# Kernel optimization log

Measured on AMD Instinct MI355X. Metric: run time of the kernel, lower is better.

Reference implementation:

```python
import jax, jax.numpy as jnp
import numpy as np

ALPHA = 0.5
N_NODES = 100000
N_EDGES = 1600000
D_IN = 128
D_OUT = 128


def setup_inputs() -> dict:
    key = jax.random.key(0)
    k1, k2, k3, k4, k5, k6 = jax.random.split(key, 6)
    x = jax.random.normal(k1, (N_NODES, D_IN), dtype=jnp.float32)
    edge_index = jax.random.randint(k2, (2, N_EDGES), 0, N_NODES, dtype=jnp.int64)
    # torch Linear default init: U(-1/sqrt(fan_in), 1/sqrt(fan_in)); scale similar here
    s = 1.0 / np.sqrt(D_IN)
    W_src = jax.random.uniform(k3, (D_OUT, D_IN), jnp.float32, -s, s)
    b_src = jax.random.uniform(k4, (D_OUT,), jnp.float32, -s, s)
    W_dst = jax.random.uniform(k5, (D_OUT, D_IN), jnp.float32, -s, s)
    b_dst = jax.random.uniform(k6, (D_OUT,), jnp.float32, -s, s)
    return {"x": x, "edge_index": edge_index, "W_src": W_src, "b_src": b_src,
            "W_dst": W_dst, "b_dst": b_dst}


def _inv_sqrt(deg):
    # deg^{-1/2} with inf -> 0 (isolated nodes)
    return jnp.where(deg > 0, jax.lax.rsqrt(jnp.maximum(deg, 1e-30)), 0.0)


def reference(x, edge_index, W_src, b_src, W_dst, b_dst):
    n = x.shape[0]
    row, col = edge_index[0], edge_index[1]
    ones = jnp.ones(row.shape[0], dtype=x.dtype)
    # degrees of directed adjacency A[row, col] = 1
    deg_out = jax.ops.segment_sum(ones, row, num_segments=n)  # row sums
    deg_in = jax.ops.segment_sum(ones, col, num_segments=n)   # col sums
    # D_out^{-1/2} A D_in^{-1/2} edge weights; transpose norm yields the SAME weights
    w = _inv_sqrt(deg_out)[row] * _inv_sqrt(deg_in)[col]      # [E]
    # adj_norm @ x : aggregate sources (col) into destinations (row)
    agg_fwd = jax.ops.segment_sum(w[:, None] * x[col], row, num_segments=n)  # [N, D_IN]
    # adj_t_norm @ x : aggregate destinations (row) into sources (col)
    agg_bwd = jax.ops.segment_sum(w[:, None] * x[row], col, num_segments=n)  # [N, D_IN]
    out = ALPHA * (agg_fwd @ W_src.T + b_src) + (1.0 - ALPHA) * (agg_bwd @ W_dst.T + b_dst)
    return out
```

## Files before the change

kernel.cpp:

```cpp
#include <hip/hip_runtime.h>
#include <stdint.h>

#define D 128
#define CE 2048
#define CAP 5120

typedef __attribute__((ext_vector_type(8))) __bf16 bf16x8;
typedef __attribute__((ext_vector_type(4))) float floatx4;

union FragU { uint4 u; bf16x8 b; };

__device__ __forceinline__ float bf16_lo(uint32_t u) { return __uint_as_float(u << 16); }
__device__ __forceinline__ float bf16_hi(uint32_t u) { return __uint_as_float(u & 0xffff0000u); }
__device__ __forceinline__ uint16_t f32_to_bf16(float f) {
    uint32_t u = __float_as_uint(f);
    uint32_t r = u + 0x7fffu + ((u >> 16) & 1u);
    return (uint16_t)(r >> 16);
}
__device__ __forceinline__ uint32_t pack2(float a, float b) {
    return (uint32_t)f32_to_bf16(a) | ((uint32_t)f32_to_bf16(b) << 16);
}

__global__ __launch_bounds__(256) void k_init(uint32_t* __restrict__ gcursor, int nb2)
{
    for (int j = threadIdx.x + blockIdx.x * 256; j < nb2; j += gridDim.x * 256)
        gcursor[j] = (uint32_t)j * CAP;
}

__global__ __launch_bounds__(256) void k_part(
    const int* __restrict__ ei, int E, int nbuk,
    uint32_t* __restrict__ gcursor, uint32_t* __restrict__ gpairs)
{
    __shared__ uint32_t cnt[1024];
    __shared__ uint32_t loff[1024];
    __shared__ uint32_t gbase[1024];
    __shared__ uint32_t spair[2 * CE];
    __shared__ uint16_t sbid[2 * CE];
    __shared__ uint32_t ssum[256];
    int nb2 = 2 * nbuk;
    for (int j = threadIdx.x; j < nb2; j += 256) cnt[j] = 0;
    __syncthreads();
    int base = blockIdx.x * CE;
    int lim = min(CE, E - base);
    for (int i = threadIdx.x; i < lim; i += 256) {
        int r = ei[base + i];
        int c = ei[E + base + i];
        atomicAdd(&cnt[r >> 8], 1u);
        atomicAdd(&cnt[nbuk + (c >> 8)], 1u);
    }
    __syncthreads();
    uint32_t v0 = 0, v1 = 0, v2 = 0, v3 = 0;
    int b0 = threadIdx.x * 4;
    if (b0 < nb2)     v0 = cnt[b0];
    if (b0 + 1 < nb2) v1 = cnt[b0 + 1];
    if (b0 + 2 < nb2) v2 = cnt[b0 + 2];
    if (b0 + 3 < nb2) v3 = cnt[b0 + 3];
    uint32_t tsum = v0 + v1 + v2 + v3;
    ssum[threadIdx.x] = tsum;
    __syncthreads();
    for (int off = 1; off < 256; off <<= 1) {
        uint32_t t = (threadIdx.x >= (unsigned)off) ? ssum[threadIdx.x - off] : 0u;
        __syncthreads();
        ssum[threadIdx.x] += t;
        __syncthreads();
    }
    uint32_t run = ssum[threadIdx.x] - tsum;
    if (b0 < nb2)     loff[b0]     = run;
    if (b0 + 1 < nb2) loff[b0 + 1] = run + v0;
    if (b0 + 2 < nb2) loff[b0 + 2] = run + v0 + v1;
    if (b0 + 3 < nb2) loff[b0 + 3] = run + v0 + v1 + v2;
    __syncthreads();
    for (int j = threadIdx.x; j < nb2; j += 256) {
        uint32_t c2 = cnt[j];
        gbase[j] = c2 ? atomicAdd(&gcursor[j], c2) : 0u;
        cnt[j] = loff[j];
    }
    __syncthreads();
    for (int i = threadIdx.x; i < lim; i += 256) {
        int r = ei[base + i];
        int c = ei[E + base + i];
        int bf = r >> 8;
        uint32_t sf = atomicAdd(&cnt[bf], 1u);
        spair[sf] = ((uint32_t)c << 8) | (uint32_t)(r & 255);
        sbid[sf] = (uint16_t)bf;
        int bb = nbuk + (c >> 8);
        uint32_t sb = atomicAdd(&cnt[bb], 1u);
        spair[sb] = ((uint32_t)r << 8) | (uint32_t)(c & 255);
        sbid[sb] = (uint16_t)bb;
    }
    __syncthreads();
    int total = 2 * lim;
    for (int s2 = threadIdx.x; s2 < total; s2 += 256) {
        int b = sbid[s2];
        gpairs[gbase[b] + ((uint32_t)s2 - loff[b])] = spair[s2];
    }
}

__global__ __launch_bounds__(256) void k_build(
    const uint32_t* __restrict__ gpairs, const uint32_t* __restrict__ gcursor,
    int nbuk, int N,
    int* __restrict__ edata, uint32_t* __restrict__ ptrg, uint32_t* __restrict__ degg,
    float* __restrict__ inv_o, float* __restrict__ inv_i)
{
    __shared__ uint32_t hist[256], cur[256], ssum[256];
    int b = blockIdx.x;
    int dir = (b >= nbuk) ? 1 : 0;
    int node0 = (b - dir * nbuk) << 8;
    uint32_t base = (uint32_t)b * CAP;
    uint32_t cnt_b = gcursor[b] - base;
    hist[threadIdx.x] = 0;
    __syncthreads();
    for (uint32_t i = threadIdx.x; i < cnt_b; i += 256)
        atomicAdd(&hist[gpairs[base + i] & 255u], 1u);
    __syncthreads();
    uint32_t h = hist[threadIdx.x];
    ssum[threadIdx.x] = h;
    __syncthreads();
    for (int off = 1; off < 256; off <<= 1) {
        uint32_t t = (threadIdx.x >= (unsigned)off) ? ssum[threadIdx.x - off] : 0u;
        __syncthreads();
        ssum[threadIdx.x] += t;
        __syncthreads();
    }
    uint32_t excl = ssum[threadIdx.x] - h;
    cur[threadIdx.x] = excl;
    int n = node0 + threadIdx.x;
    if (n < N) {
        ptrg[dir * N + n] = base + excl;
        degg[dir * N + n] = h;
        float iv = h ? rsqrtf((float)h) : 0.0f;
        if (dir == 0) inv_o[n] = iv; else inv_i[n] = iv;
    }
    __syncthreads();
    for (uint32_t i = threadIdx.x; i < cnt_b; i += 256) {
        uint32_t e = gpairs[base + i];
        uint32_t pos = atomicAdd(&cur[e & 255u], 1u);
        edata[base + pos] = (int)(e >> 8);
    }
}

__global__ __launch_bounds__(256) void k_mm(
    const float* __restrict__ x,
    const float* __restrict__ Wsrc, const float* __restrict__ Wdst,
    const float* __restrict__ inv_o, const float* __restrict__ inv_i,
    uint32_t* __restrict__ u2, uint32_t* __restrict__ v2, int N)
{
    __shared__ uint4 sWf[2048];
    const int lane = threadIdx.x & 63;
    const int m16 = lane & 15;
    const int quad = lane >> 4;
    const int mat = blockIdx.x & 1;
    uint32_t* outb = mat ? v2 : u2;
    const float* inv = mat ? inv_o : inv_i;
    const float* Wm = mat ? Wdst : Wsrc;

    {
        uint32_t* sW32 = (uint32_t*)sWf;
        for (int idx = threadIdx.x; idx < 8192; idx += 256) {
            int slot = idx >> 2, j2 = idx & 3;
            int ct = slot >> 8, ks = (slot >> 6) & 3, qd = (slot >> 4) & 3, mm = slot & 15;
            const float2 w = *(const float2*)(Wm + (ct * 16 + mm) * 128 + ks * 32 + qd * 8 + 2 * j2);
            sW32[idx] = pack2(0.5f * w.x, 0.5f * w.y);
        }
    }
    __syncthreads();

    const int ntiles = (N + 15) >> 4;
    const int wslot = (blockIdx.x >> 1) * 4 + (threadIdx.x >> 6);
    const int nslot = (gridDim.x >> 1) * 4;

    for (int t = wslot; t < ntiles; t += nslot) {
        int node = t * 16 + m16;
        int rowA = node < N ? node : N - 1;
        const float4* xr = (const float4*)(x + (long)rowA * 128);
        bf16x8 Xf[4];
        #pragma unroll
        for (int ks = 0; ks < 4; ++ks) {
            float4 p0 = xr[ks * 8 + quad * 2];
            float4 p1 = xr[ks * 8 + quad * 2 + 1];
            FragU f;
            f.u.x = pack2(p0.x, p0.y);
            f.u.y = pack2(p0.z, p0.w);
            f.u.z = pack2(p1.x, p1.y);
            f.u.w = pack2(p1.z, p1.w);
            Xf[ks] = f.b;
        }
        float iv = inv[rowA];
        bool ok = (node < N);
        #pragma unroll
        for (int ct = 0; ct < 8; ++ct) {
            floatx4 acc = {};
            #pragma unroll
            for (int ks = 0; ks < 4; ++ks) {
                FragU wf; wf.u = sWf[ct * 256 + ks * 64 + lane];
                acc = __builtin_amdgcn_mfma_f32_16x16x32_bf16(wf.b, Xf[ks], acc, 0, 0, 0);
            }
            if (ok) {
                uint2 val;
                val.x = pack2(acc[0] * iv, acc[1] * iv);
                val.y = pack2(acc[2] * iv, acc[3] * iv);
                *(uint2*)(outb + (long)node * 64 + ct * 8 + quad * 2) = val;
            }
        }
    }
}

__global__ __launch_bounds__(256) void k_gather(
    const uint32_t* __restrict__ u2, const uint32_t* __restrict__ v2,
    const int* __restrict__ edata,
    const uint32_t* __restrict__ ptrg, const uint32_t* __restrict__ degg,
    const float* __restrict__ inv_out, const float* __restrict__ inv_in,
    const float* __restrict__ bsrc, const float* __restrict__ bdst,
    float2* __restrict__ out2, int N, int nStart, int nEnd)
{
    int lane = threadIdx.x & 63;
    int node = nStart + blockIdx.x * 4 + (threadIdx.x >> 6);
    if (node >= nEnd) return;

    uint32_t s0 = ptrg[node],     d0 = degg[node];
    uint32_t s1 = ptrg[N + node], d1 = degg[N + node];

    float fx = 0, fy = 0, bx = 0, by = 0;
    uint32_t k = 0;
    for (; k + 4 <= d0; k += 4) {
        uint32_t p0 = u2[(long)edata[s0 + k]     * 64 + lane];
        uint32_t p1 = u2[(long)edata[s0 + k + 1] * 64 + lane];
        uint32_t p2 = u2[(long)edata[s0 + k + 2] * 64 + lane];
        uint32_t p3 = u2[(long)edata[s0 + k + 3] * 64 + lane];
        fx += bf16_lo(p0) + bf16_lo(p1) + bf16_lo(p2) + bf16_lo(p3);
        fy += bf16_hi(p0) + bf16_hi(p1) + bf16_hi(p2) + bf16_hi(p3);
    }
    for (; k < d0; ++k) {
        uint32_t p = u2[(long)edata[s0 + k] * 64 + lane];
        fx += bf16_lo(p); fy += bf16_hi(p);
    }
    k = 0;
    for (; k + 4 <= d1; k += 4) {
        uint32_t p0 = v2[(long)edata[s1 + k]     * 64 + lane];
        uint32_t p1 = v2[(long)edata[s1 + k + 1] * 64 + lane];
        uint32_t p2 = v2[(long)edata[s1 + k + 2] * 64 + lane];
        uint32_t p3 = v2[(long)edata[s1 + k + 3] * 64 + lane];
        bx += bf16_lo(p0) + bf16_lo(p1) + bf16_lo(p2) + bf16_lo(p3);
        by += bf16_hi(p0) + bf16_hi(p1) + bf16_hi(p2) + bf16_hi(p3);
    }
    for (; k < d1; ++k) {
        uint32_t p = v2[(long)edata[s1 + k] * 64 + lane];
        bx += bf16_lo(p); by += bf16_hi(p);
    }

    float io = inv_out[node], ii = inv_in[node];
    float b0 = 0.5f * (bsrc[2 * lane]     + bdst[2 * lane]);
    float b1 = 0.5f * (bsrc[2 * lane + 1] + bdst[2 * lane + 1]);
    out2[(long)node * 64 + lane] =
        make_float2(io * fx + ii * bx + b0, io * fy + ii * by + b1);
}

extern "C" void kernel_launch(void* const* d_in, const int* in_sizes, int n_in,
                              void* d_out, int out_size, void* d_ws, size_t ws_size,
                              hipStream_t stream) {
    const int N = in_sizes[0] / D;
    const int E = in_sizes[1] / 2;
    const int nbuk = (N + 255) >> 8;
    const int nb2 = 2 * nbuk;

    const float* x    = (const float*)d_in[0];
    const int*   ei   = (const int*)d_in[1];
    const float* Wsrc = (const float*)d_in[2];
    const float* bsrc = (const float*)d_in[3];
    const float* Wdst = (const float*)d_in[4];
    const float* bdst = (const float*)d_in[5];

    char* ws = (char*)d_ws;
    size_t off = 0;
    uint32_t* gcur   = (uint32_t*)(ws + off); off += 1024 * 4;
    float*    inv_o  = (float*)(ws + off);    off += (size_t)N * 4;
    float*    inv_i  = (float*)(ws + off);    off += (size_t)N * 4;
    uint32_t* ptrg   = (uint32_t*)(ws + off); off += (size_t)2 * N * 4;
    uint32_t* degg   = (uint32_t*)(ws + off); off += (size_t)2 * N * 4;
    uint32_t* gpairs = (uint32_t*)(ws + off); off += (size_t)nb2 * CAP * 4;
    int*      edata  = (int*)(ws + off);      off += (size_t)nb2 * CAP * 4;
    uint32_t* u2     = (uint32_t*)(ws + off); off += (size_t)N * 64 * 4;
    uint32_t* v2     = (uint32_t*)(ws + off); off += (size_t)N * 64 * 4;

    k_init<<<4, 256, 0, stream>>>(gcur, nb2);

    k_part<<<(E + CE - 1) / CE, 256, 0, stream>>>(ei, E, nbuk, gcur, gpairs);

    k_build<<<nb2, 256, 0, stream>>>(gpairs, gcur, nbuk, N,
                                     edata, ptrg, degg, inv_o, inv_i);

    k_mm<<<2048, 256, 0, stream>>>(x, Wsrc, Wdst, inv_o, inv_i, u2, v2, N);

    int half = (N + 1) / 2;
    k_gather<<<(half + 3) / 4, 256, 0, stream>>>(u2, v2, edata, ptrg, degg,
                                                 inv_o, inv_i, bsrc, bdst,
                                                 (float2*)d_out, N, 0, half);
    k_gather<<<(N - half + 3) / 4, 256, 0, stream>>>(u2, v2, edata, ptrg, degg,
                                                     inv_o, inv_i, bsrc, bdst,
                                                     (float2*)d_out, N, half, N);
}
```

Measured before the change: 347.7 us.

## Precompute bf16 weight fragments once and split matmul and gather launches

```diff
diff --git a/kernel.cpp b/kernel.cpp
--- a/kernel.cpp
+++ b/kernel.cpp
@@ -12,13 +12,22 @@
 
 __device__ __forceinline__ float bf16_lo(uint32_t u) { return __uint_as_float(u << 16); }
 __device__ __forceinline__ float bf16_hi(uint32_t u) { return __uint_as_float(u & 0xffff0000u); }
-__device__ __forceinline__ uint16_t f32_to_bf16(float f) {
-    uint32_t u = __float_as_uint(f);
-    uint32_t r = u + 0x7fffu + ((u >> 16) & 1u);
-    return (uint16_t)(r >> 16);
-}
 __device__ __forceinline__ uint32_t pack2(float a, float b) {
-    return (uint32_t)f32_to_bf16(a) | ((uint32_t)f32_to_bf16(b) << 16);
+    return ((__float_as_uint(a) + 0x8000u) >> 16) | ((__float_as_uint(b) + 0x8000u) & 0xffff0000u);
+}
+
+__global__ __launch_bounds__(256) void k_prep_w(
+    const float* __restrict__ Wsrc, const float* __restrict__ Wdst,
+    uint32_t* __restrict__ Wfrag)
+{
+    int idx = blockIdx.x * 256 + threadIdx.x;
+    int mat = idx >> 13;
+    int id2 = idx & 8191;
+    int slot = id2 >> 2, j2 = id2 & 3;
+    int ct = slot >> 8, ks = (slot >> 6) & 3, qd = (slot >> 4) & 3, mm = slot & 15;
+    const float* Wm = mat ? Wdst : Wsrc;
+    const float2 w = *(const float2*)(Wm + (ct * 16 + mm) * 128 + ks * 32 + qd * 8 + 2 * j2);
+    Wfrag[idx] = pack2(0.5f * w.x, 0.5f * w.y);
 }
 
 __global__ __launch_bounds__(256) void k_init(uint32_t* __restrict__ gcursor, int nb2)
@@ -140,34 +149,20 @@
 }
 
 __global__ __launch_bounds__(256) void k_mm(
-    const float* __restrict__ x,
-    const float* __restrict__ Wsrc, const float* __restrict__ Wdst,
-    const float* __restrict__ inv_o, const float* __restrict__ inv_i,
-    uint32_t* __restrict__ u2, uint32_t* __restrict__ v2, int N)
+    const float* __restrict__ x, const uint4* __restrict__ wf,
+    const float* __restrict__ inv, uint32_t* __restrict__ outb, int N)
 {
     __shared__ uint4 sWf[2048];
+    for (int i = threadIdx.x; i < 2048; i += 256) sWf[i] = wf[i];
+    __syncthreads();
+
     const int lane = threadIdx.x & 63;
     const int m16 = lane & 15;
     const int quad = lane >> 4;
-    const int mat = blockIdx.x & 1;
-    uint32_t* outb = mat ? v2 : u2;
-    const float* inv = mat ? inv_o : inv_i;
-    const float* Wm = mat ? Wdst : Wsrc;
-
-    {
-        uint32_t* sW32 = (uint32_t*)sWf;
-        for (int idx = threadIdx.x; idx < 8192; idx += 256) {
-            int slot = idx >> 2, j2 = idx & 3;
-            int ct = slot >> 8, ks = (slot >> 6) & 3, qd = (slot >> 4) & 3, mm = slot & 15;
-            const float2 w = *(const float2*)(Wm + (ct * 16 + mm) * 128 + ks * 32 + qd * 8 + 2 * j2);
-            sW32[idx] = pack2(0.5f * w.x, 0.5f * w.y);
-        }
-    }
-    __syncthreads();
 
     const int ntiles = (N + 15) >> 4;
-    const int wslot = (blockIdx.x >> 1) * 4 + (threadIdx.x >> 6);
-    const int nslot = (gridDim.x >> 1) * 4;
+    const int wslot = blockIdx.x * 4 + (threadIdx.x >> 6);
+    const int nslot = gridDim.x * 4;
 
     for (int t = wslot; t < ntiles; t += nslot) {
         int node = t * 16 + m16;
@@ -192,8 +187,8 @@
             floatx4 acc = {};
             #pragma unroll
             for (int ks = 0; ks < 4; ++ks) {
-                FragU wf; wf.u = sWf[ct * 256 + ks * 64 + lane];
-                acc = __builtin_amdgcn_mfma_f32_16x16x32_bf16(wf.b, Xf[ks], acc, 0, 0, 0);
+                FragU wfr; wfr.u = sWf[ct * 256 + ks * 64 + lane];
+                acc = __builtin_amdgcn_mfma_f32_16x16x32_bf16(wfr.b, Xf[ks], acc, 0, 0, 0);
             }
             if (ok) {
                 uint2 val;
@@ -273,6 +268,7 @@
     char* ws = (char*)d_ws;
     size_t off = 0;
     uint32_t* gcur   = (uint32_t*)(ws + off); off += 1024 * 4;
+    uint32_t* wfrag  = (uint32_t*)(ws + off); off += 16384 * 4;
     float*    inv_o  = (float*)(ws + off);    off += (size_t)N * 4;
     float*    inv_i  = (float*)(ws + off);    off += (size_t)N * 4;
     uint32_t* ptrg   = (uint32_t*)(ws + off); off += (size_t)2 * N * 4;
@@ -282,6 +278,8 @@
     uint32_t* u2     = (uint32_t*)(ws + off); off += (size_t)N * 64 * 4;
     uint32_t* v2     = (uint32_t*)(ws + off); off += (size_t)N * 64 * 4;
 
+    k_prep_w<<<64, 256, 0, stream>>>(Wsrc, Wdst, wfrag);
+
     k_init<<<4, 256, 0, stream>>>(gcur, nb2);
 
     k_part<<<(E + CE - 1) / CE, 256, 0, stream>>>(ei, E, nbuk, gcur, gpairs);
@@ -289,13 +287,17 @@
     k_build<<<nb2, 256, 0, stream>>>(gpairs, gcur, nbuk, N,
                                      edata, ptrg, degg, inv_o, inv_i);
 
-    k_mm<<<2048, 256, 0, stream>>>(x, Wsrc, Wdst, inv_o, inv_i, u2, v2, N);
-
-    int half = (N + 1) / 2;
-    k_gather<<<(half + 3) / 4, 256, 0, stream>>>(u2, v2, edata, ptrg, degg,
-                                                 inv_o, inv_i, bsrc, bdst,
-                                                 (float2*)d_out, N, 0, half);
-    k_gather<<<(N - half + 3) / 4, 256, 0, stream>>>(u2, v2, edata, ptrg, degg,
-                                                     inv_o, inv_i, bsrc, bdst,
-                                                     (float2*)d_out, N, half, N);
-}
+    k_mm<<<640, 256, 0, stream>>>(x, (const uint4*)wfrag,        inv_i, u2, N);
+    k_mm<<<640, 256, 0, stream>>>(x, (const uint4*)(wfrag + 8192), inv_o, v2, N);
+
+    int c1 = (N + 2) / 3, c2 = 2 * c1;
+    k_gather<<<(c1 + 3) / 4, 256, 0, stream>>>(u2, v2, edata, ptrg, degg,
+                                               inv_o, inv_i, bsrc, bdst,
+                                               (float2*)d_out, N, 0, c1);
+    k_gather<<<(c1 + 3) / 4, 256, 0, stream>>>(u2, v2, edata, ptrg, degg,
+                                               inv_o, inv_i, bsrc, bdst,
+                                               (float2*)d_out, N, c1, c2);
+    k_gather<<<(N - c2 + 3) / 4, 256, 0, stream>>>(u2, v2, edata, ptrg, degg,
+                                                   inv_o, inv_i, bsrc, bdst,
+                                                   (float2*)d_out, N, c2, N);
+}
```

New measurement: 351.9 us. No clear change (+1.2%).
